# Performance work log

Hardware: AMD Instinct MI355X
Metric: run time of the kernel (lower is better)

## Reference

```python
import jax, jax.numpy as jnp
import numpy as np

L, D, H, DR, KF = 2, 256, 8, 64, 4   # n_layer, d_model, n_head, d_rpe, k_feedforward
B, S, T = 2, 256, 256
LN_EPS = 1e-5


def _ln(x, g, b):
    m = jnp.mean(x, -1, keepdims=True)
    v = jnp.mean((x - m) ** 2, -1, keepdims=True)
    return (x - m) * jax.lax.rsqrt(v + LN_EPS) * g + b


def _attn_rpe(q_in, kv_in, rpe, tgt_mask, wq, bq, wk, bk, wv, bv, wo, bo, wr, br):
    # RPE-biased multi-head cross attention: rpe -> (rpe_k, rpe_v) added per (src,tgt) pair.
    Bq, Sq, _ = q_in.shape
    Tk = kv_in.shape[1]
    Dh = D // H
    q = (q_in @ wq + bq).reshape(Bq, Sq, H, Dh)
    k = (kv_in @ wk + bk).reshape(Bq, Tk, H, Dh)
    v = (kv_in @ wv + bv).reshape(Bq, Tk, H, Dh)
    r = rpe @ wr + br                                   # [B,S,T,2D]
    rk, rv = jnp.split(r, 2, axis=-1)
    rk = rk.reshape(Bq, Sq, Tk, H, Dh)
    rv = rv.reshape(Bq, Sq, Tk, H, Dh)
    scale = 1.0 / np.sqrt(Dh).astype(np.float32)
    scores = (jnp.einsum('bshd,bthd->bhst', q, k)
              + jnp.einsum('bshd,bsthd->bhst', q, rk)) * scale
    scores = jnp.where(tgt_mask[:, None, None, :], -jnp.inf, scores)
    w = jax.nn.softmax(scores, axis=-1)                 # [B,H,S,T]
    out = (jnp.einsum('bhst,bthd->bshd', w, v)
           + jnp.einsum('bhst,bsthd->bshd', w, rv))
    return out.reshape(Bq, Sq, D) @ wo + bo


def _forward(src, tgt, rpe, src_padding_mask, tgt_padding_mask, p):
    for i in range(L):  # loop over n_layer (structurally distinct params)
        s2 = _ln(src, p['ln1_g'][i], p['ln1_b'][i])
        tn = _ln(tgt, p['lnt_g'][i], p['lnt_b'][i])
        a = _attn_rpe(s2, tn, rpe, tgt_padding_mask,
                      p['wq'][i], p['bq'][i], p['wk'][i], p['bk'][i],
                      p['wv'][i], p['bv'][i], p['wo'][i], p['bo'][i],
                      p['wr'][i], p['br'][i])
        src = src + a
        s2 = _ln(src, p['ln2_g'][i], p['ln2_b'][i])
        s2 = jax.nn.relu(s2 @ p['w1'][i] + p['b1'][i]) @ p['w2'][i] + p['b2'][i]
        src = src + s2
        src = jnp.where(src_padding_mask[:, :, None], 0.0, src)
    return src


def setup_inputs() -> dict:
    key = jax.random.key(0)
    ks = jax.random.split(key, 16)
    f = lambda k, shp: (0.02 * jax.random.normal(k, shp)).astype(jnp.float32)
    return {
        'src': jax.random.normal(ks[0], (B, S, D), jnp.float32),
        'tgt': jax.random.normal(ks[1], (B, T, D), jnp.float32),
        'rpe': jax.random.normal(ks[2], (B, S, T, DR), jnp.float32),
        'src_padding_mask': jax.random.bernoulli(ks[3], 0.05, (B, S)),
        'tgt_padding_mask': jax.random.bernoulli(ks[4], 0.1, (B, T)),
        'ln1_g': jnp.ones((L, D), jnp.float32), 'ln1_b': jnp.zeros((L, D), jnp.float32),
        'lnt_g': jnp.ones((L, D), jnp.float32), 'lnt_b': jnp.zeros((L, D), jnp.float32),
        'ln2_g': jnp.ones((L, D), jnp.float32), 'ln2_b': jnp.zeros((L, D), jnp.float32),
        'wq': f(ks[5], (L, D, D)), 'bq': jnp.zeros((L, D), jnp.float32),
        'wk': f(ks[6], (L, D, D)), 'bk': jnp.zeros((L, D), jnp.float32),
        'wv': f(ks[7], (L, D, D)), 'bv': jnp.zeros((L, D), jnp.float32),
        'wo': f(ks[8], (L, D, D)), 'bo': jnp.zeros((L, D), jnp.float32),
        'wr': f(ks[9], (L, DR, 2 * D)), 'br': jnp.zeros((L, 2 * D), jnp.float32),
        'w1': f(ks[10], (L, D, KF * D)), 'b1': jnp.zeros((L, KF * D), jnp.float32),
        'w2': f(ks[11], (L, KF * D, D)), 'b2': jnp.zeros((L, D), jnp.float32),
    }


def reference(src, tgt, rpe, src_padding_mask, tgt_padding_mask,
              ln1_g, ln1_b, lnt_g, lnt_b, ln2_g, ln2_b,
              wq, bq, wk, bk, wv, bv, wo, bo, wr, br, w1, b1, w2, b2):
    p = dict(ln1_g=ln1_g, ln1_b=ln1_b, lnt_g=lnt_g, lnt_b=lnt_b,
             ln2_g=ln2_g, ln2_b=ln2_b, wq=wq, bq=bq, wk=wk, bk=bk,
             wv=wv, bv=bv, wo=wo, bo=bo, wr=wr, br=br,
             w1=w1, b1=b1, w2=w2, b2=b2)
    return _forward(src, tgt, rpe, src_padding_mask, tgt_padding_mask, p)
```

## Files before the change

kernel.cpp:

```cpp
#include <hip/hip_runtime.h>
#include <math.h>

#define NEG_INF -1e30f

__global__ __launch_bounds__(256) void qkv_ln_kernel(
    const float* __restrict__ srcin, const float* __restrict__ tgt,
    const float* __restrict__ g1, const float* __restrict__ b1,
    const float* __restrict__ gt, const float* __restrict__ bt,
    const float* __restrict__ bo,
    const float* __restrict__ wq, const float* __restrict__ wk, const float* __restrict__ wv,
    const float* __restrict__ bq, const float* __restrict__ bk, const float* __restrict__ bv,
    float* __restrict__ Qb, float* __restrict__ Kb, float* __restrict__ Vb,
    float* __restrict__ X)
{
  __shared__ float As[32][8][36];
  __shared__ float Bs[32][36];
  int z = blockIdx.z;
  int m0 = blockIdx.y * 32, n0 = blockIdx.x * 32;
  const float* Bw   = (z == 0) ? wq : (z == 1) ? wk : wv;
  const float* bias = (z == 0) ? bq : (z == 1) ? bk : bv;
  const float* g    = (z == 0) ? g1 : gt;
  const float* be   = (z == 0) ? b1 : bt;
  int tid = threadIdx.x;
  int r = tid >> 3, c8 = tid & 7;
  int row = m0 + r;
  const float* arow = ((z == 0) ? srcin : tgt) + (size_t)row * 256 + c8 * 32;

  float4 x[8];
  float s = 0, ss = 0;
#pragma unroll
  for (int j = 0; j < 8; ++j) {
    x[j] = ((const float4*)arow)[j];
    s  += x[j].x + x[j].y + x[j].z + x[j].w;
    ss += x[j].x*x[j].x + x[j].y*x[j].y + x[j].z*x[j].z + x[j].w*x[j].w;
  }
#pragma unroll
  for (int off = 1; off < 8; off <<= 1) {
    s  += __shfl_xor(s,  off);
    ss += __shfl_xor(ss, off);
  }
  float mean = s * (1.0f / 256.0f);
  float var  = ss * (1.0f / 256.0f) - mean * mean;
  float rstd = rsqrtf(var + 1e-5f);
#pragma unroll
  for (int j = 0; j < 8; ++j) {
    float4 gg = ((const float4*)(g  + c8 * 32))[j];
    float4 bb = ((const float4*)(be + c8 * 32))[j];
    As[j*4+0][c8][r] = (x[j].x - mean) * rstd * gg.x + bb.x;
    As[j*4+1][c8][r] = (x[j].y - mean) * rstd * gg.y + bb.y;
    As[j*4+2][c8][r] = (x[j].z - mean) * rstd * gg.z + bb.z;
    As[j*4+3][c8][r] = (x[j].w - mean) * rstd * gg.w + bb.w;
  }
  if (z == 0 && blockIdx.x == 0) {
#pragma unroll
    for (int j = 0; j < 8; ++j) {
      float4 bo4 = ((const float4*)(bo + c8 * 32))[j];
      float4 xi;
      xi.x = x[j].x + bo4.x; xi.y = x[j].y + bo4.y;
      xi.z = x[j].z + bo4.z; xi.w = x[j].w + bo4.w;
      *(float4*)&X[(size_t)row * 256 + c8 * 32 + j * 4] = xi;
    }
  }
  __syncthreads();

  int tx = tid & 15, ty = tid >> 4;
  float acc[2][2] = {};
  for (int kc = 0; kc < 256; kc += 32) {
    float4 b0 = *(const float4*)(Bw + (size_t)(kc + r) * 256 + n0 + c8 * 4);
    *(float4*)&Bs[r][c8 * 4] = b0;
    __syncthreads();
    int kcc = kc >> 5;
#pragma unroll
    for (int kk = 0; kk < 32; ++kk) {
      float2 av = *(const float2*)&As[kk][kcc][ty * 2];
      float2 bv = *(const float2*)&Bs[kk][tx * 2];
      acc[0][0] = fmaf(av.x, bv.x, acc[0][0]); acc[0][1] = fmaf(av.x, bv.y, acc[0][1]);
      acc[1][0] = fmaf(av.y, bv.x, acc[1][0]); acc[1][1] = fmaf(av.y, bv.y, acc[1][1]);
    }
    __syncthreads();
  }

  int c0 = n0 + tx * 2;
  const float scale = 0.1767766952966369f;
#pragma unroll
  for (int i = 0; i < 2; ++i) {
    int m = m0 + ty * 2 + i;
    float2 rr;
    rr.x = acc[i][0] + bias[c0 + 0];
    rr.y = acc[i][1] + bias[c0 + 1];
    if (z == 0) {
      rr.x *= scale; rr.y *= scale;
      *(float2*)&Qb[m * 256 + c0] = rr;
    } else {
      int b = m >> 8, t = m & 255, h = c0 >> 5, d0 = c0 & 31;
      float* dst = ((z == 1) ? Kb : Vb) + (size_t)(b * 8 + h) * 8192 + t * 32 + d0;
      *(float2*)dst = rr;
    }
  }
}

__global__ __launch_bounds__(256) void ff1_ln2_kernel(
    const float* __restrict__ Xin,
    const float* __restrict__ g2, const float* __restrict__ be2,
    const float* __restrict__ b2, const int* __restrict__ smask,
    const float* __restrict__ w1, const float* __restrict__ b1,
    float* __restrict__ H1, float* __restrict__ outb)
{
  __shared__ float As[32][8][36];
  __shared__ float Bs[32][36];
  int m0 = blockIdx.y * 32, n0 = blockIdx.x * 32;
  int tid = threadIdx.x;
  int r = tid >> 3, c8 = tid & 7;
  int row = m0 + r;
  const float* arow = Xin + (size_t)row * 256 + c8 * 32;

  float4 x[8];
  float s = 0, ss = 0;
#pragma unroll
  for (int j = 0; j < 8; ++j) {
    x[j] = ((const float4*)arow)[j];
    s  += x[j].x + x[j].y + x[j].z + x[j].w;
    ss += x[j].x*x[j].x + x[j].y*x[j].y + x[j].z*x[j].z + x[j].w*x[j].w;
  }
#pragma unroll
  for (int off = 1; off < 8; off <<= 1) {
    s  += __shfl_xor(s,  off);
    ss += __shfl_xor(ss, off);
  }
  float mean = s * (1.0f / 256.0f);
  float var  = ss * (1.0f / 256.0f) - mean * mean;
  float rstd = rsqrtf(var + 1e-5f);
#pragma unroll
  for (int j = 0; j < 8; ++j) {
    float4 gg = ((const float4*)(g2  + c8 * 32))[j];
    float4 bb = ((const float4*)(be2 + c8 * 32))[j];
    As[j*4+0][c8][r] = (x[j].x - mean) * rstd * gg.x + bb.x;
    As[j*4+1][c8][r] = (x[j].y - mean) * rstd * gg.y + bb.y;
    As[j*4+2][c8][r] = (x[j].z - mean) * rstd * gg.z + bb.z;
    As[j*4+3][c8][r] = (x[j].w - mean) * rstd * gg.w + bb.w;
  }
  if (blockIdx.x == 0) {
    float mm = (smask[row] != 0) ? 0.0f : 1.0f;
#pragma unroll
    for (int j = 0; j < 8; ++j) {
      float4 b24 = ((const float4*)(b2 + c8 * 32))[j];
      float4 oi;
      oi.x = mm * (x[j].x + b24.x); oi.y = mm * (x[j].y + b24.y);
      oi.z = mm * (x[j].z + b24.z); oi.w = mm * (x[j].w + b24.w);
      *(float4*)&outb[(size_t)row * 256 + c8 * 32 + j * 4] = oi;
    }
  }
  __syncthreads();

  int tx = tid & 15, ty = tid >> 4;
  float acc[2][2] = {};
  for (int kc = 0; kc < 256; kc += 32) {
    float4 b0 = *(const float4*)(w1 + (size_t)(kc + r) * 1024 + n0 + c8 * 4);
    *(float4*)&Bs[r][c8 * 4] = b0;
    __syncthreads();
    int kcc = kc >> 5;
#pragma unroll
    for (int kk = 0; kk < 32; ++kk) {
      float2 av = *(const float2*)&As[kk][kcc][ty * 2];
      float2 bv = *(const float2*)&Bs[kk][tx * 2];
      acc[0][0] = fmaf(av.x, bv.x, acc[0][0]); acc[0][1] = fmaf(av.x, bv.y, acc[0][1]);
      acc[1][0] = fmaf(av.y, bv.x, acc[1][0]); acc[1][1] = fmaf(av.y, bv.y, acc[1][1]);
    }
    __syncthreads();
  }

  int c0 = n0 + tx * 2;
#pragma unroll
  for (int i = 0; i < 2; ++i) {
    int m = m0 + ty * 2 + i;
    float2 rr;
    rr.x = fmaxf(acc[i][0] + b1[c0 + 0], 0.0f);
    rr.y = fmaxf(acc[i][1] + b1[c0 + 1], 0.0f);
    *(float2*)&H1[m * 1024 + c0] = rr;
  }
}

__device__ __forceinline__ void gemm_core32x32(
    const float* __restrict__ A, int lda,
    const float* __restrict__ Bw, int ldb,
    int kbeg, int kend, int m0, int n0,
    float acc[2][2])
{
  __shared__ float At[32][36];
  __shared__ float Bs[32][36];
  int tid = threadIdx.x;
  int tx = tid & 15, ty = tid >> 4;
  int r  = tid >> 3, c8 = tid & 7;
  for (int kc = kbeg; kc < kend; kc += 32) {
    float4 a  = *(const float4*)(A  + (size_t)(m0 + r) * lda + kc + c8 * 4);
    float4 b0 = *(const float4*)(Bw + (size_t)(kc + r) * ldb + n0 + c8 * 4);
    At[c8*4+0][r] = a.x; At[c8*4+1][r] = a.y; At[c8*4+2][r] = a.z; At[c8*4+3][r] = a.w;
    *(float4*)&Bs[r][c8 * 4] = b0;
    __syncthreads();
#pragma unroll
    for (int k = 0; k < 32; ++k) {
      float2 av = *(const float2*)&At[k][ty * 2];
      float2 bv = *(const float2*)&Bs[k][tx * 2];
      acc[0][0] = fmaf(av.x, bv.x, acc[0][0]); acc[0][1] = fmaf(av.x, bv.y, acc[0][1]);
      acc[1][0] = fmaf(av.y, bv.x, acc[1][0]); acc[1][1] = fmaf(av.y, bv.y, acc[1][1]);
    }
    __syncthreads();
  }
}

__global__ __launch_bounds__(256) void wo_kernel(
    const float* __restrict__ AO, const float* __restrict__ wo,
    float* __restrict__ X)
{
  int m0 = blockIdx.y * 32, n0 = blockIdx.x * 32;
  int kbeg = blockIdx.z * 128;
  float acc[2][2] = {};
  gemm_core32x32(AO, 256, wo, 256, kbeg, kbeg + 128, m0, n0, acc);
  int tid = threadIdx.x, tx = tid & 15, ty = tid >> 4;
  int c0 = n0 + tx * 2;
#pragma unroll
  for (int i = 0; i < 2; ++i) {
    int m = m0 + ty * 2 + i;
    atomicAdd(&X[m * 256 + c0 + 0], acc[i][0]);
    atomicAdd(&X[m * 256 + c0 + 1], acc[i][1]);
  }
}

__global__ __launch_bounds__(256) void ff2_kernel(
    const float* __restrict__ H1, const float* __restrict__ w2,
    const int* __restrict__ smask, float* __restrict__ outb)
{
  int m0 = blockIdx.y * 32, n0 = blockIdx.x * 32;
  int kbeg = blockIdx.z * 256;
  float acc[2][2] = {};
  gemm_core32x32(H1, 1024, w2, 256, kbeg, kbeg + 256, m0, n0, acc);
  int tid = threadIdx.x, tx = tid & 15, ty = tid >> 4;
  int c0 = n0 + tx * 2;
#pragma unroll
  for (int i = 0; i < 2; ++i) {
    int m = m0 + ty * 2 + i;
    float mm = (smask[m] != 0) ? 0.0f : 1.0f;
    atomicAdd(&outb[m * 256 + c0 + 0], mm * acc[i][0]);
    atomicAdd(&outb[m * 256 + c0 + 1], mm * acc[i][1]);
  }
}

__global__ __launch_bounds__(256) void attn_kernel(
    const float* __restrict__ Qb, const float* __restrict__ Kb, const float* __restrict__ Vb,
    const float* __restrict__ rpe, const int* __restrict__ tmask,
    const float* __restrict__ wrl, const float* __restrict__ brl,
    float* __restrict__ AO)
{
  __shared__ float Ks[256][32];
  __shared__ float Vt[32][260];
  __shared__ float ps[4][256];
  __shared__ float qs[8][32];
  __shared__ float wks[5][32];
  __shared__ float wvs[5][32];
  int bid = blockIdx.x;
  int b = bid >> 8, h = (bid >> 5) & 7, s0 = (bid & 31) << 3;
  int tid = threadIdx.x;
  const float* Kp = Kb + (size_t)(b * 8 + h) * 8192;
  const float* Vp = Vb + (size_t)(b * 8 + h) * 8192;
  {
    int t = tid;
    const float4* kr = (const float4*)(Kp + t * 32);
    const float4* vr = (const float4*)(Vp + t * 32);
    int sw = t & 7;
#pragma unroll
    for (int c = 0; c < 8; ++c) {
      float4 k4 = kr[c];
      *(float4*)&Ks[t][(c ^ sw) * 4] = k4;
    }
#pragma unroll
    for (int c = 0; c < 8; ++c) {
      float4 v4 = vr[c];
      Vt[c*4+0][t] = v4.x; Vt[c*4+1][t] = v4.y; Vt[c*4+2][t] = v4.z; Vt[c*4+3][t] = v4.w;
    }
  }
  if (tid < 160) {
    int j = tid >> 5, d = tid & 31;
    wks[j][d] = (j < 4) ? wrl[j * 512 + h * 32 + d]       : brl[h * 32 + d];
    wvs[j][d] = (j < 4) ? wrl[j * 512 + 256 + h * 32 + d] : brl[256 + h * 32 + d];
  }
  if (tid >= 192) {
    int u = tid - 192;
    int rr2 = u >> 3, cc = u & 7;
    *(float4*)&qs[rr2][cc*4] =
        *(const float4*)&Qb[(b * 256 + s0 + rr2) * 256 + h * 32 + cc * 4];
  }
  __syncthreads();

  int w = tid >> 6, lane = tid & 63;
  int msk[4];
#pragma unroll
  for (int it = 0; it < 4; ++it) msk[it] = tmask[b * 256 + it * 64 + lane];

  for (int i = 0; i < 2; ++i) {
    int sl = w * 2 + i;
    int s = s0 + sl;
    float4 q4[8];
#pragma unroll
    for (int c = 0; c < 8; ++c) q4[c] = *(const float4*)&qs[sl][c * 4];
    float qw[4]; float qbr = 0.0f;
#pragma unroll
    for (int j = 0; j < 4; ++j) {
      float t0 = 0;
#pragma unroll
      for (int c = 0; c < 8; ++c) {
        float4 wv4 = *(const float4*)&wks[j][c * 4];
        t0 += q4[c].x*wv4.x + q4[c].y*wv4.y + q4[c].z*wv4.z + q4[c].w*wv4.w;
      }
      qw[j] = t0;
    }
#pragma unroll
    for (int c = 0; c < 8; ++c) {
      float4 wv4 = *(const float4*)&wks[4][c * 4];
      qbr += q4[c].x*wv4.x + q4[c].y*wv4.y + q4[c].z*wv4.z + q4[c].w*wv4.w;
    }
    const float4* rp4 = (const float4*)(rpe + (size_t)(b * 256 + s) * 1024);
    float sc[4]; float4 rr[4];
#pragma unroll
    for (int it = 0; it < 4; ++it) {
      int t = it * 64 + lane;
      int sw = t & 7;
      float sv = 0;
#pragma unroll
      for (int c = 0; c < 8; ++c) {
        float4 k4 = *(const float4*)&Ks[t][(c ^ sw) * 4];
        sv = fmaf(q4[c].x, k4.x, sv); sv = fmaf(q4[c].y, k4.y, sv);
        sv = fmaf(q4[c].z, k4.z, sv); sv = fmaf(q4[c].w, k4.w, sv);
      }
      float4 rv = rp4[t];
      rr[it] = rv;
      sv += rv.x*qw[0] + rv.y*qw[1] + rv.z*qw[2] + rv.w*qw[3] + qbr;
      if (msk[it] != 0) sv = NEG_INF;
      sc[it] = sv;
    }
    float mval = fmaxf(fmaxf(sc[0], sc[1]), fmaxf(sc[2], sc[3]));
#pragma unroll
    for (int off = 32; off >= 1; off >>= 1) mval = fmaxf(mval, __shfl_xor(mval, off));
    float p[4], lsum = 0;
#pragma unroll
    for (int it = 0; it < 4; ++it) { p[it] = __expf(sc[it] - mval); lsum += p[it]; }
    float wj0 = 0, wj1 = 0, wj2 = 0, wj3 = 0;
#pragma unroll
    for (int it = 0; it < 4; ++it) {
      wj0 = fmaf(p[it], rr[it].x, wj0);
      wj1 = fmaf(p[it], rr[it].y, wj1);
      wj2 = fmaf(p[it], rr[it].z, wj2);
      wj3 = fmaf(p[it], rr[it].w, wj3);
    }
#pragma unroll
    for (int off = 32; off >= 1; off >>= 1) {
      lsum += __shfl_xor(lsum, off);
      wj0 += __shfl_xor(wj0, off);
      wj1 += __shfl_xor(wj1, off);
      wj2 += __shfl_xor(wj2, off);
      wj3 += __shfl_xor(wj3, off);
    }
#pragma unroll
    for (int it = 0; it < 4; ++it) ps[w][it * 64 + lane] = p[it];
    int g = lane >> 5, d = lane & 31;
    float o = 0;
#pragma unroll
    for (int n = 0; n < 32; ++n) {
      int t = g * 128 + n * 4;
      float4 p4 = *(const float4*)&ps[w][t];
      float4 v4 = *(const float4*)&Vt[d][t];
      o += p4.x*v4.x + p4.y*v4.y + p4.z*v4.z + p4.w*v4.w;
    }
    o += __shfl_xor(o, 32);
    float corr = wj0 * wvs[0][d] + wj1 * wvs[1][d] + wj2 * wvs[2][d] + wj3 * wvs[3][d];
    float oval = (o + corr) / lsum + wvs[4][d];
    if (lane < 32) AO[(b * 256 + s) * 256 + h * 32 + d] = oval;
  }
}

extern "C" void kernel_launch(void* const* d_in, const int* in_sizes, int n_in,
                              void* d_out, int out_size, void* d_ws, size_t ws_size,
                              hipStream_t stream)
{
  const float* src  = (const float*)d_in[0];
  const float* tgt  = (const float*)d_in[1];
  const float* rpe  = (const float*)d_in[2];
  const int*   smask = (const int*)d_in[3];
  const int*   tmask = (const int*)d_in[4];
  const float* ln1g = (const float*)d_in[5];
  const float* ln1b = (const float*)d_in[6];
  const float* lntg = (const float*)d_in[7];
  const float* lntb = (const float*)d_in[8];
  const float* ln2g = (const float*)d_in[9];
  const float* ln2b = (const float*)d_in[10];
  const float* wq = (const float*)d_in[11];
  const float* bq = (const float*)d_in[12];
  const float* wk = (const float*)d_in[13];
  const float* bk = (const float*)d_in[14];
  const float* wv = (const float*)d_in[15];
  const float* bv = (const float*)d_in[16];
  const float* wo = (const float*)d_in[17];
  const float* bo = (const float*)d_in[18];
  const float* wr = (const float*)d_in[19];
  const float* br = (const float*)d_in[20];
  const float* w1 = (const float*)d_in[21];
  const float* b1 = (const float*)d_in[22];
  const float* w2 = (const float*)d_in[23];
  const float* b2 = (const float*)d_in[24];

  float* ws   = (float*)d_ws;
  float* Qb   = ws;
  float* Kb   = ws + 131072;
  float* Vb   = ws + 262144;
  float* AO   = ws + 393216;
  float* X    = ws + 524288;
  float* SRC1 = ws + 655360;
  float* H1   = ws + 786432;

  for (int l = 0; l < 2; ++l) {
    const float* srcin = l ? SRC1 : src;
    float* outb = l ? (float*)d_out : SRC1;
    qkv_ln_kernel<<<dim3(8, 16, 3), 256, 0, stream>>>(
        srcin, tgt, ln1g + l*256, ln1b + l*256, lntg + l*256, lntb + l*256,
        bo + l*256,
        wq + l*65536, wk + l*65536, wv + l*65536,
        bq + l*256, bk + l*256, bv + l*256,
        Qb, Kb, Vb, X);
    attn_kernel<<<512, 256, 0, stream>>>(Qb, Kb, Vb, rpe, tmask,
                                         wr + l*2048, br + l*512, AO);
    wo_kernel<<<dim3(8, 16, 2), 256, 0, stream>>>(AO, wo + l*65536, X);
    ff1_ln2_kernel<<<dim3(32, 16), 256, 0, stream>>>(
        X, ln2g + l*256, ln2b + l*256, b2 + l*256, smask,
        w1 + l*262144, b1 + l*1024, H1, outb);
    ff2_kernel<<<dim3(8, 16, 4), 256, 0, stream>>>(H1, w2 + l*262144, smask, outb);
  }
}
```

Before: 274.2 us.

## Stage full K-range of GEMM operands in shared memory with a single barrier

The small GEMM kernels (QKV, FF1, Wo, FF2) now load the whole K-slice of the B operand, and for Wo/FF2 also the A operand, into shared memory up front. This issues all global loads together and needs only one barrier, where before there were two barriers per 32-wide K chunk. The cost is much larger shared memory per block (up to about 70 KB for ff2), which may cap occupancy. Launch bounds now request 2 blocks per SIMD/CU.

```diff
diff --git a/kernel.cpp b/kernel.cpp
--- a/kernel.cpp
+++ b/kernel.cpp
@@ -3,7 +3,7 @@
 
 #define NEG_INF -1e30f
 
-__global__ __launch_bounds__(256) void qkv_ln_kernel(
+__global__ __launch_bounds__(256, 2) void qkv_ln_kernel(
     const float* __restrict__ srcin, const float* __restrict__ tgt,
     const float* __restrict__ g1, const float* __restrict__ b1,
     const float* __restrict__ gt, const float* __restrict__ bt,
@@ -14,7 +14,7 @@
     float* __restrict__ X)
 {
   __shared__ float As[32][8][36];
-  __shared__ float Bs[32][36];
+  __shared__ float Bs[256][34];
   int z = blockIdx.z;
   int m0 = blockIdx.y * 32, n0 = blockIdx.x * 32;
   const float* Bw   = (z == 0) ? wq : (z == 1) ? wk : wv;
@@ -51,6 +51,12 @@
     As[j*4+2][c8][r] = (x[j].z - mean) * rstd * gg.z + bb.z;
     As[j*4+3][c8][r] = (x[j].w - mean) * rstd * gg.w + bb.w;
   }
+#pragma unroll
+  for (int kb = 0; kb < 8; ++kb) {
+    int k = kb * 32 + r;
+    float4 b4 = *(const float4*)(Bw + (size_t)k * 256 + n0 + c8 * 4);
+    *(float4*)&Bs[k][c8 * 4] = b4;
+  }
   if (z == 0 && blockIdx.x == 0) {
 #pragma unroll
     for (int j = 0; j < 8; ++j) {
@@ -65,19 +71,14 @@
 
   int tx = tid & 15, ty = tid >> 4;
   float acc[2][2] = {};
-  for (int kc = 0; kc < 256; kc += 32) {
-    float4 b0 = *(const float4*)(Bw + (size_t)(kc + r) * 256 + n0 + c8 * 4);
-    *(float4*)&Bs[r][c8 * 4] = b0;
-    __syncthreads();
-    int kcc = kc >> 5;
+  for (int kcc = 0; kcc < 8; ++kcc) {
 #pragma unroll
     for (int kk = 0; kk < 32; ++kk) {
       float2 av = *(const float2*)&As[kk][kcc][ty * 2];
-      float2 bv = *(const float2*)&Bs[kk][tx * 2];
+      float2 bv = *(const float2*)&Bs[kcc * 32 + kk][tx * 2];
       acc[0][0] = fmaf(av.x, bv.x, acc[0][0]); acc[0][1] = fmaf(av.x, bv.y, acc[0][1]);
       acc[1][0] = fmaf(av.y, bv.x, acc[1][0]); acc[1][1] = fmaf(av.y, bv.y, acc[1][1]);
     }
-    __syncthreads();
   }
 
   int c0 = n0 + tx * 2;
@@ -99,7 +100,7 @@
   }
 }
 
-__global__ __launch_bounds__(256) void ff1_ln2_kernel(
+__global__ __launch_bounds__(256, 2) void ff1_ln2_kernel(
     const float* __restrict__ Xin,
     const float* __restrict__ g2, const float* __restrict__ be2,
     const float* __restrict__ b2, const int* __restrict__ smask,
@@ -107,7 +108,7 @@
     float* __restrict__ H1, float* __restrict__ outb)
 {
   __shared__ float As[32][8][36];
-  __shared__ float Bs[32][36];
+  __shared__ float Bs[256][34];
   int m0 = blockIdx.y * 32, n0 = blockIdx.x * 32;
   int tid = threadIdx.x;
   int r = tid >> 3, c8 = tid & 7;
@@ -139,6 +140,12 @@
     As[j*4+2][c8][r] = (x[j].z - mean) * rstd * gg.z + bb.z;
     As[j*4+3][c8][r] = (x[j].w - mean) * rstd * gg.w + bb.w;
   }
+#pragma unroll
+  for (int kb = 0; kb < 8; ++kb) {
+    int k = kb * 32 + r;
+    float4 b4 = *(const float4*)(w1 + (size_t)k * 1024 + n0 + c8 * 4);
+    *(float4*)&Bs[k][c8 * 4] = b4;
+  }
   if (blockIdx.x == 0) {
     float mm = (smask[row] != 0) ? 0.0f : 1.0f;
 #pragma unroll
@@ -154,19 +161,14 @@
 
   int tx = tid & 15, ty = tid >> 4;
   float acc[2][2] = {};
-  for (int kc = 0; kc < 256; kc += 32) {
-    float4 b0 = *(const float4*)(w1 + (size_t)(kc + r) * 1024 + n0 + c8 * 4);
-    *(float4*)&Bs[r][c8 * 4] = b0;
-    __syncthreads();
-    int kcc = kc >> 5;
+  for (int kcc = 0; kcc < 8; ++kcc) {
 #pragma unroll
     for (int kk = 0; kk < 32; ++kk) {
       float2 av = *(const float2*)&As[kk][kcc][ty * 2];
-      float2 bv = *(const float2*)&Bs[kk][tx * 2];
+      float2 bv = *(const float2*)&Bs[kcc * 32 + kk][tx * 2];
       acc[0][0] = fmaf(av.x, bv.x, acc[0][0]); acc[0][1] = fmaf(av.x, bv.y, acc[0][1]);
       acc[1][0] = fmaf(av.y, bv.x, acc[1][0]); acc[1][1] = fmaf(av.y, bv.y, acc[1][1]);
     }
-    __syncthreads();
   }
 
   int c0 = n0 + tx * 2;
@@ -180,42 +182,52 @@
   }
 }
 
-__device__ __forceinline__ void gemm_core32x32(
+template<int KPASS>
+__device__ __forceinline__ void gemm_full32(
     const float* __restrict__ A, int lda,
     const float* __restrict__ Bw, int ldb,
-    int kbeg, int kend, int m0, int n0,
+    int kbeg, int m0, int n0,
+    float* At , float* Bs ,
     float acc[2][2])
 {
-  __shared__ float At[32][36];
-  __shared__ float Bs[32][36];
   int tid = threadIdx.x;
+  int r = tid >> 3, c8 = tid & 7;
+#pragma unroll
+  for (int kb = 0; kb < KPASS; ++kb) {
+    int kl = kb * 32 + c8 * 4;
+    float4 a4 = *(const float4*)(A + (size_t)(m0 + r) * lda + kbeg + kl);
+    At[(kl + 0) * 34 + r] = a4.x;
+    At[(kl + 1) * 34 + r] = a4.y;
+    At[(kl + 2) * 34 + r] = a4.z;
+    At[(kl + 3) * 34 + r] = a4.w;
+    int k = kb * 32 + r;
+    float4 b4 = *(const float4*)(Bw + (size_t)(kbeg + k) * ldb + n0 + c8 * 4);
+    *(float4*)&Bs[k * 34 + c8 * 4] = b4;
+  }
+  __syncthreads();
   int tx = tid & 15, ty = tid >> 4;
-  int r  = tid >> 3, c8 = tid & 7;
-  for (int kc = kbeg; kc < kend; kc += 32) {
-    float4 a  = *(const float4*)(A  + (size_t)(m0 + r) * lda + kc + c8 * 4);
-    float4 b0 = *(const float4*)(Bw + (size_t)(kc + r) * ldb + n0 + c8 * 4);
-    At[c8*4+0][r] = a.x; At[c8*4+1][r] = a.y; At[c8*4+2][r] = a.z; At[c8*4+3][r] = a.w;
-    *(float4*)&Bs[r][c8 * 4] = b0;
-    __syncthreads();
-#pragma unroll
-    for (int k = 0; k < 32; ++k) {
-      float2 av = *(const float2*)&At[k][ty * 2];
-      float2 bv = *(const float2*)&Bs[k][tx * 2];
+  for (int kc = 0; kc < KPASS; ++kc) {
+#pragma unroll
+    for (int kk = 0; kk < 32; ++kk) {
+      int k = kc * 32 + kk;
+      float2 av = *(const float2*)&At[k * 34 + ty * 2];
+      float2 bv = *(const float2*)&Bs[k * 34 + tx * 2];
       acc[0][0] = fmaf(av.x, bv.x, acc[0][0]); acc[0][1] = fmaf(av.x, bv.y, acc[0][1]);
       acc[1][0] = fmaf(av.y, bv.x, acc[1][0]); acc[1][1] = fmaf(av.y, bv.y, acc[1][1]);
     }
-    __syncthreads();
-  }
-}
-
-__global__ __launch_bounds__(256) void wo_kernel(
+  }
+}
+
+__global__ __launch_bounds__(256, 2) void wo_kernel(
     const float* __restrict__ AO, const float* __restrict__ wo,
     float* __restrict__ X)
 {
+  __shared__ float At[128 * 34];
+  __shared__ float Bs[128 * 34];
   int m0 = blockIdx.y * 32, n0 = blockIdx.x * 32;
   int kbeg = blockIdx.z * 128;
   float acc[2][2] = {};
-  gemm_core32x32(AO, 256, wo, 256, kbeg, kbeg + 128, m0, n0, acc);
+  gemm_full32<4>(AO, 256, wo, 256, kbeg, m0, n0, At, Bs, acc);
   int tid = threadIdx.x, tx = tid & 15, ty = tid >> 4;
   int c0 = n0 + tx * 2;
 #pragma unroll
@@ -226,14 +238,16 @@
   }
 }
 
-__global__ __launch_bounds__(256) void ff2_kernel(
+__global__ __launch_bounds__(256, 2) void ff2_kernel(
     const float* __restrict__ H1, const float* __restrict__ w2,
     const int* __restrict__ smask, float* __restrict__ outb)
 {
+  __shared__ float At[256 * 34];
+  __shared__ float Bs[256 * 34];
   int m0 = blockIdx.y * 32, n0 = blockIdx.x * 32;
   int kbeg = blockIdx.z * 256;
   float acc[2][2] = {};
-  gemm_core32x32(H1, 1024, w2, 256, kbeg, kbeg + 256, m0, n0, acc);
+  gemm_full32<8>(H1, 1024, w2, 256, kbeg, m0, n0, At, Bs, acc);
   int tid = threadIdx.x, tx = tid & 15, ty = tid >> 4;
   int c0 = n0 + tx * 2;
 #pragma unroll
```

After: 267.7 us. 1.02x faster.
